# Kernel tuning notes

Measured on AMD Instinct MI355X. Metric: run time of the kernel, lower is better.

## Reference

```python
import jax, jax.numpy as jnp
import numpy as np

Q_DIM, KV_DIM, N_HEAD, C, OUT_DIM, N_AXIS = 256, 256, 8, 32, 256, 1
B, S = 1, 2048

def setup_inputs() -> dict:
    key = jax.random.key(0)
    ks = jax.random.split(key, 9)
    sd = 0.05
    return {
        "q_inputs": jax.random.normal(ks[0], (B, S, Q_DIM), jnp.float32),
        "kv_inputs": jax.random.normal(ks[1], (B, S, KV_DIM), jnp.float32),
        "bias": jax.random.normal(ks[2], (B, N_HEAD, S, S), jnp.float32),
        "qg_weights": jax.random.normal(ks[3], (Q_DIM, N_AXIS, N_HEAD, 2 * C), jnp.float32) * sd,
        "kv_weights": jax.random.normal(ks[4], (KV_DIM, N_AXIS, N_HEAD, 2 * C), jnp.float32) * sd,
        "qg_bias": jax.random.normal(ks[5], (N_AXIS, N_HEAD, 1, 2 * C), jnp.float32) * sd,
        "kv_bias": jax.random.normal(ks[6], (N_AXIS, N_HEAD, 1, 2 * C), jnp.float32) * sd,
        "o_weights": jax.random.normal(ks[7], (N_AXIS, N_HEAD, C, OUT_DIM), jnp.float32) * sd,
        "o_bias": jax.random.normal(ks[8], (OUT_DIM, N_AXIS), jnp.float32) * sd,
    }

def reference(q_inputs, kv_inputs, bias, qg_weights, kv_weights, qg_bias, kv_bias, o_weights, o_bias):
    scale = C ** (-0.5)
    # to_unsqueeze path: add axis dim r (=n_axis=1)
    qi = q_inputs[..., None]          # (B, q, q_dim, r)
    ki = kv_inputs[..., None]         # (B, k, kv_dim, r)
    b = bias[:, None]                 # (B, 1, h, q, k) broadcasts over r
    # per-axis, per-head QKV projections with bias
    qg = jnp.einsum('bqar,arhc->brhqc', qi, qg_weights) + qg_bias
    q, g = jnp.split(qg, 2, axis=-1)  # (B, r, h, q, c) each
    kv = jnp.einsum('bkar,arhc->brhkc', ki, kv_weights) + kv_bias
    k, v = jnp.split(kv, 2, axis=-1)  # (B, r, h, k, c) each
    logits = jnp.einsum('brhqc,brhkc->brhqk', q * scale, k) + b
    attn = jax.nn.softmax(logits, axis=-1)
    attn_out = jnp.einsum('brhqk,brhkc->brhqc', attn, v)
    attn_out = attn_out * jax.nn.sigmoid(g)  # gating
    output = jnp.einsum('brhqc,rhco->bqor', attn_out, o_weights) + o_bias
    return output[..., 0]  # squeeze the n_axis dim (to_unsqueeze path)
```

## Files before the change

### kernel.cpp

```cpp
#include <hip/hip_runtime.h>
#include <hip/hip_bf16.h>
#include <math.h>

#define SEQ   2048
#define NHEAD 8

typedef __attribute__((ext_vector_type(8))) short bf16x8;
typedef __attribute__((ext_vector_type(4))) short bf16x4;
typedef __attribute__((ext_vector_type(4))) float f32x4;

static __device__ __forceinline__ short f2bf(float f) {
    __hip_bfloat16 h = __float2bfloat16(f);
    return *reinterpret_cast<short*>(&h);
}

__global__ __launch_bounds__(256)
void prep_w_kernel(const float* __restrict__ qg_w, const float* __restrict__ kv_w,
                   const float* __restrict__ o_w, short* __restrict__ wqgT,
                   short* __restrict__ wkvT, short* __restrict__ owT)
{
    __shared__ float t[64][65];
    int bid = blockIdx.x;
    const float* src; short* dst; int N, tr, tc;
    if (bid < 32)      { src = qg_w; dst = wqgT; N = 512; tr = bid >> 3; tc = bid & 7; }
    else if (bid < 64) { bid -= 32; src = kv_w; dst = wkvT; N = 512; tr = bid >> 3; tc = bid & 7; }
    else               { bid -= 64; src = o_w;  dst = owT;  N = 256; tr = bid >> 2; tc = bid & 3; }

    const int tid = threadIdx.x;
    const int rr = tid >> 6;
    const int cc = tid & 63;
#pragma unroll
    for (int s = 0; s < 16; s++)
        t[(s << 2) + rr][cc] =
            src[(size_t)((tr << 6) + (s << 2) + rr) * N + (tc << 6) + cc];
    __syncthreads();
#pragma unroll
    for (int s = 0; s < 16; s++)
        dst[(size_t)((tc << 6) + (s << 2) + rr) * 256 + (tr << 6) + cc]
            = f2bf(t[cc][(s << 2) + rr]);
}

__global__ __launch_bounds__(256)
void proj_qgkv_kernel(const float* __restrict__ q_in, const float* __restrict__ kv_in,
                      const short* __restrict__ wqgT, const short* __restrict__ wkvT,
                      const float* __restrict__ qg_b, const float* __restrict__ kv_b,
                      short* __restrict__ qs, float* __restrict__ gs,
                      short* __restrict__ ks, short* __restrict__ vT)
{
    const int z = blockIdx.z;
    const float* __restrict__ A  = z ? kv_in : q_in;
    const short* __restrict__ W  = z ? wkvT : wqgT;
    const float* __restrict__ bv = z ? kv_b : qg_b;

    const int tid = threadIdx.x;
    const int wq = tid >> 6, lane = tid & 63;
    const int ln = lane & 15, quad = lane >> 4;
    const int m0 = blockIdx.x << 6;
    const int n0 = blockIdx.y << 5;

    f32x4 acc[2];
#pragma unroll
    for (int nt = 0; nt < 2; nt++) {
        const float b = bv[n0 + (nt << 4) + ln];
        acc[nt] = (f32x4){b, b, b, b};
    }

    const float* ap = A + (size_t)(m0 + (wq << 4) + ln) * 256 + (quad << 3);
    for (int k8 = 0; k8 < 8; k8++) {
        float4 a0 = *(const float4*)(ap + (k8 << 5));
        float4 a1 = *(const float4*)(ap + (k8 << 5) + 4);
        bf16x8 a;
        a[0] = f2bf(a0.x); a[1] = f2bf(a0.y); a[2] = f2bf(a0.z); a[3] = f2bf(a0.w);
        a[4] = f2bf(a1.x); a[5] = f2bf(a1.y); a[6] = f2bf(a1.z); a[7] = f2bf(a1.w);
#pragma unroll
        for (int nt = 0; nt < 2; nt++) {
            bf16x8 b = *(const bf16x8*)(W + (size_t)(n0 + (nt << 4) + ln) * 256
                                          + (k8 << 5) + (quad << 3));
            acc[nt] = __builtin_amdgcn_mfma_f32_16x16x32_bf16(a, b, acc[nt], 0, 0, 0);
        }
    }

    const float scale = 0.17677669529663689f;
#pragma unroll
    for (int nt = 0; nt < 2; nt++) {
        const int n = n0 + (nt << 4) + ln;
        const int h = n >> 6, c2 = n & 63;
#pragma unroll
        for (int r = 0; r < 4; r++) {
            const int m = m0 + (wq << 4) + (quad << 2) + r;
            const float v = acc[nt][r];
            if (z == 0) {
                if (c2 < 32) qs[(((h << 11) + m) << 5) + c2] = f2bf(v * scale);
                else gs[(((h << 11) + m) << 5) + (c2 - 32)] = 1.0f / (1.0f + __expf(-v));
            } else {
                if (c2 < 32) ks[(((h << 11) + m) << 5) + c2] = f2bf(v);
                else vT[(((h << 5) + (c2 - 32)) << 11) + m] = f2bf(v);
            }
        }
    }
}

__global__ __launch_bounds__(256, 6)
void attn_kernel(const short* __restrict__ qs, const short* __restrict__ ks,
                 const short* __restrict__ vT, const float* __restrict__ bias,
                 float* __restrict__ Opart, float* __restrict__ mpart,
                 float* __restrict__ lpart, int ksize)
{
    const int h = blockIdx.y, z = blockIdx.z;
    const int q0 = blockIdx.x << 6;
    const int tid = threadIdx.x;
    const int wq = tid >> 6, lane = tid & 63;
    const int ln = lane & 15, quad = lane >> 4;

    const int qrow = q0 + (wq << 4) + ln;
    const bf16x8 qf = *(const bf16x8*)(qs + (((size_t)(h << 11) + qrow) << 5) + (quad << 3));

    const float L2E = 1.44269504088896f;
    float ml2 = -1e30f, l = 0.f;
    f32x4 O0 = {0, 0, 0, 0}, O1 = {0, 0, 0, 0};

    const int kbeg  = z * ksize;
    const int ntile = ksize >> 6;
    const float* bp = bias + ((size_t)h * SEQ + qrow) * SEQ + kbeg + (quad << 2);
    const short* kp = ks + (((size_t)(h << 11) + kbeg + ln) << 5) + (quad << 3);

    for (int kt = 0; kt < ntile; kt++) {
        const int k0 = kbeg + (kt << 6);

        f32x4 cb[4];
#pragma unroll
        for (int mt = 0; mt < 4; mt++)
            cb[mt] = *(const f32x4*)(bp + (kt << 6) + (mt << 4));
        bf16x8 kf[4];
#pragma unroll
        for (int mt = 0; mt < 4; mt++)
            kf[mt] = *(const bf16x8*)(kp + (size_t)(((kt << 6) + (mt << 4)) << 5));
        bf16x4 vh[2][2][2];
#pragma unroll
        for (int cm = 0; cm < 2; cm++) {
            const size_t vb = (((size_t)(h << 5) + (cm << 4) + ln) << 11) + k0 + (quad << 2);
#pragma unroll
            for (int kc = 0; kc < 2; kc++)
#pragma unroll
                for (int hf = 0; hf < 2; hf++)
                    vh[cm][kc][hf] = *(const bf16x4*)(vT + vb + (kc << 5) + (hf << 4));
        }

        f32x4 S[4];
#pragma unroll
        for (int mt = 0; mt < 4; mt++)
            S[mt] = __builtin_amdgcn_mfma_f32_16x16x32_bf16(kf[mt], qf, cb[mt], 0, 0, 0);

        float smax = S[0][0];
#pragma unroll
        for (int mt = 0; mt < 4; mt++)
#pragma unroll
            for (int r = 0; r < 4; r++) smax = fmaxf(smax, S[mt][r]);
        smax = fmaxf(smax, __shfl_xor(smax, 16));
        smax = fmaxf(smax, __shfl_xor(smax, 32));
        const float mnew = fmaxf(ml2, smax * L2E);
        const float alpha = exp2f(ml2 - mnew);
        ml2 = mnew;

        float pr[4][4];
        float rs = 0.f;
#pragma unroll
        for (int mt = 0; mt < 4; mt++)
#pragma unroll
            for (int r = 0; r < 4; r++) {
                const float p = exp2f(fmaf(S[mt][r], L2E, -mnew));
                pr[mt][r] = p;
                rs += p;
            }
        rs += __shfl_xor(rs, 16);
        rs += __shfl_xor(rs, 32);
        l = l * alpha + rs;

        short pb[4][4];
#pragma unroll
        for (int mt = 0; mt < 4; mt++)
#pragma unroll
            for (int r = 0; r < 4; r++) pb[mt][r] = f2bf(pr[mt][r]);
        bf16x8 P0 = {pb[0][0], pb[0][1], pb[0][2], pb[0][3],
                     pb[1][0], pb[1][1], pb[1][2], pb[1][3]};
        bf16x8 P1 = {pb[2][0], pb[2][1], pb[2][2], pb[2][3],
                     pb[3][0], pb[3][1], pb[3][2], pb[3][3]};

        O0 *= alpha;
        O1 *= alpha;
#pragma unroll
        for (int kc = 0; kc < 2; kc++) {
            const bf16x8 P = kc ? P1 : P0;
            bf16x8 va0 = __builtin_shufflevector(vh[0][kc][0], vh[0][kc][1],
                                                 0, 1, 2, 3, 4, 5, 6, 7);
            bf16x8 va1 = __builtin_shufflevector(vh[1][kc][0], vh[1][kc][1],
                                                 0, 1, 2, 3, 4, 5, 6, 7);
            O0 = __builtin_amdgcn_mfma_f32_16x16x32_bf16(va0, P, O0, 0, 0, 0);
            O1 = __builtin_amdgcn_mfma_f32_16x16x32_bf16(va1, P, O1, 0, 0, 0);
        }
    }

    const size_t pb_ = (((size_t)(z * NHEAD + h)) << 11) + qrow;
    if (quad == 0) { mpart[pb_] = ml2; lpart[pb_] = l; }
    float* op = Opart + (pb_ << 5);
#pragma unroll
    for (int r = 0; r < 4; r++) {
        op[(quad << 2) + r]      = O0[r];
        op[16 + (quad << 2) + r] = O1[r];
    }
}

__global__ __launch_bounds__(256)
void combine_kernel(const float* __restrict__ Opart, const float* __restrict__ mpart,
                    const float* __restrict__ lpart, const float* __restrict__ gs,
                    short* __restrict__ att, int nsplit)
{
    const int g  = blockIdx.x * 256 + threadIdx.x;
    const int c4 = g & 7;
    const int q  = (g >> 3) & (SEQ - 1);
    const int h  = g >> 14;

    float M = -1e30f;
    for (int s = 0; s < nsplit; s++)
        M = fmaxf(M, mpart[(((size_t)s * NHEAD + h) << 11) + q]);

    float l = 0.f;
    float4 O = {0.f, 0.f, 0.f, 0.f};
    for (int s = 0; s < nsplit; s++) {
        const size_t base = (((size_t)s * NHEAD + h) << 11) + q;
        const float w = exp2f(mpart[base] - M);
        l += w * lpart[base];
        float4 o4 = *(const float4*)(Opart + (base << 5) + (c4 << 2));
        O.x = fmaf(w, o4.x, O.x); O.y = fmaf(w, o4.y, O.y);
        O.z = fmaf(w, o4.z, O.z); O.w = fmaf(w, o4.w, O.w);
    }
    const float inv = 1.0f / l;
    float4 g4 = *(const float4*)(gs + ((((size_t)h << 11) + q) << 5) + (c4 << 2));
    bf16x4 r;
    r[0] = f2bf(O.x * inv * g4.x); r[1] = f2bf(O.y * inv * g4.y);
    r[2] = f2bf(O.z * inv * g4.z); r[3] = f2bf(O.w * inv * g4.w);
    *(bf16x4*)(att + ((size_t)q << 8) + (h << 5) + (c4 << 2)) = r;
}

__global__ __launch_bounds__(256)
void proj_o_kernel(const short* __restrict__ att, const short* __restrict__ owT,
                   const float* __restrict__ o_b, float* __restrict__ out)
{
    const int tid = threadIdx.x;
    const int wq = tid >> 6, lane = tid & 63;
    const int ln = lane & 15, quad = lane >> 4;
    const int m0 = blockIdx.x << 6;
    const int n0 = blockIdx.y << 4;

    const int n = n0 + ln;
    const float b = o_b[n];
    f32x4 acc = (f32x4){b, b, b, b};

    const short* ap = att + (size_t)(m0 + (wq << 4) + ln) * 256 + (quad << 3);
    const short* bp = owT + (size_t)n * 256 + (quad << 3);
#pragma unroll
    for (int k8 = 0; k8 < 8; k8++) {
        bf16x8 a = *(const bf16x8*)(ap + (k8 << 5));
        bf16x8 w = *(const bf16x8*)(bp + (k8 << 5));
        acc = __builtin_amdgcn_mfma_f32_16x16x32_bf16(a, w, acc, 0, 0, 0);
    }
#pragma unroll
    for (int r = 0; r < 4; r++) {
        const int m = m0 + (wq << 4) + (quad << 2) + r;
        out[(size_t)m * 256 + n] = acc[r];
    }
}

extern "C" void kernel_launch(void* const* d_in, const int* in_sizes, int n_in,
                              void* d_out, int out_size, void* d_ws, size_t ws_size,
                              hipStream_t stream)
{
    const float* q_in  = (const float*)d_in[0];
    const float* kv_in = (const float*)d_in[1];
    const float* bias  = (const float*)d_in[2];
    const float* qg_w  = (const float*)d_in[3];
    const float* kv_w  = (const float*)d_in[4];
    const float* qg_b  = (const float*)d_in[5];
    const float* kv_b  = (const float*)d_in[6];
    const float* o_w   = (const float*)d_in[7];
    const float* o_b   = (const float*)d_in[8];
    float* out = (float*)d_out;

    char* p = (char*)d_ws;
    short* qs   = (short*)p; p += 1048576;
    short* ksb  = (short*)p; p += 1048576;
    short* vTb  = (short*)p; p += 1048576;
    short* attb = (short*)p; p += 1048576;
    short* wqgT = (short*)p; p += 262144;
    short* wkvT = (short*)p; p += 262144;
    short* owT  = (short*)p; p += 131072;
    float* gs   = (float*)p; p += 2097152;

    const size_t fixed = (size_t)(p - (char*)d_ws);
    int nsplit = 1;
    {
        const int cand[4] = {8, 4, 2, 1};
        for (int i = 0; i < 4; i++) {
            size_t ns = (size_t)cand[i];
            if (fixed + ns * (size_t)(2097152 + 2 * 65536) <= ws_size) {
                nsplit = cand[i]; break;
            }
        }
    }
    float* mp = (float*)p;
    float* lp = mp + (size_t)nsplit * NHEAD * SEQ;
    float* Op = lp + (size_t)nsplit * NHEAD * SEQ;

    hipLaunchKernelGGL(prep_w_kernel, dim3(80), dim3(256), 0, stream,
                       qg_w, kv_w, o_w, wqgT, wkvT, owT);
    hipLaunchKernelGGL(proj_qgkv_kernel, dim3(32, 16, 2), dim3(256), 0, stream,
                       q_in, kv_in, wqgT, wkvT, qg_b, kv_b, qs, gs, ksb, vTb);
    hipLaunchKernelGGL(attn_kernel, dim3(32, NHEAD, nsplit), dim3(256), 0, stream,
                       qs, ksb, vTb, bias, Op, mp, lp, SEQ / nsplit);
    hipLaunchKernelGGL(combine_kernel, dim3(512), dim3(256), 0, stream,
                       Op, mp, lp, gs, attb, nsplit);
    hipLaunchKernelGGL(proj_o_kernel, dim3(32, 16), dim3(256), 0, stream,
                       attb, owT, o_b, out);
}
```

Baseline: 263.5 us.

## Double-buffer attention loads and pre-pack V into MFMA-fragment layout

The projection kernel now writes V in a packed per-tile layout matching the MFMA operand fragments, so the attention kernel loads V with single 16-byte loads instead of 4-element pieces plus shuffles. The attention loop is templated on tile count and fully unrolled, with register double-buffering of bias, K and V for the next tile, and occupancy hints reduced to 3 blocks to make room for the extra registers. The projection GEMMs also gain register double-buffered loads and vectorized output stores. The aim is to hide global load latency on the bias stream, which dominates memory traffic, at the cost of higher register pressure and lower occupancy.

```diff
diff --git a/kernel.cpp b/kernel.cpp
--- a/kernel.cpp
+++ b/kernel.cpp
@@ -40,12 +40,12 @@
             = f2bf(t[cc][(s << 2) + rr]);
 }
 
-__global__ __launch_bounds__(256)
+__global__ __launch_bounds__(256, 4)
 void proj_qgkv_kernel(const float* __restrict__ q_in, const float* __restrict__ kv_in,
                       const short* __restrict__ wqgT, const short* __restrict__ wkvT,
                       const float* __restrict__ qg_b, const float* __restrict__ kv_b,
                       short* __restrict__ qs, float* __restrict__ gs,
-                      short* __restrict__ ks, short* __restrict__ vT)
+                      short* __restrict__ ks, short* __restrict__ vP)
 {
     const int z = blockIdx.z;
     const float* __restrict__ A  = z ? kv_in : q_in;
@@ -66,18 +66,27 @@
     }
 
     const float* ap = A + (size_t)(m0 + (wq << 4) + ln) * 256 + (quad << 3);
+    const short* wp = W + (size_t)(n0 + ln) * 256 + (quad << 3);
+
+    float4 a4[2][2]; bf16x8 wb[2][2];
+    auto ldp = [&](int b, int k8) {
+        a4[b][0] = *(const float4*)(ap + (k8 << 5));
+        a4[b][1] = *(const float4*)(ap + (k8 << 5) + 4);
+        wb[b][0] = *(const bf16x8*)(wp + (k8 << 5));
+        wb[b][1] = *(const bf16x8*)(wp + 4096 + (k8 << 5));
+    };
+    ldp(0, 0);
+#pragma unroll
     for (int k8 = 0; k8 < 8; k8++) {
-        float4 a0 = *(const float4*)(ap + (k8 << 5));
-        float4 a1 = *(const float4*)(ap + (k8 << 5) + 4);
+        const int b = k8 & 1;
+        if (k8 < 7) ldp(b ^ 1, k8 + 1);
         bf16x8 a;
-        a[0] = f2bf(a0.x); a[1] = f2bf(a0.y); a[2] = f2bf(a0.z); a[3] = f2bf(a0.w);
-        a[4] = f2bf(a1.x); a[5] = f2bf(a1.y); a[6] = f2bf(a1.z); a[7] = f2bf(a1.w);
-#pragma unroll
-        for (int nt = 0; nt < 2; nt++) {
-            bf16x8 b = *(const bf16x8*)(W + (size_t)(n0 + (nt << 4) + ln) * 256
-                                          + (k8 << 5) + (quad << 3));
-            acc[nt] = __builtin_amdgcn_mfma_f32_16x16x32_bf16(a, b, acc[nt], 0, 0, 0);
-        }
+        a[0] = f2bf(a4[b][0].x); a[1] = f2bf(a4[b][0].y);
+        a[2] = f2bf(a4[b][0].z); a[3] = f2bf(a4[b][0].w);
+        a[4] = f2bf(a4[b][1].x); a[5] = f2bf(a4[b][1].y);
+        a[6] = f2bf(a4[b][1].z); a[7] = f2bf(a4[b][1].w);
+        acc[0] = __builtin_amdgcn_mfma_f32_16x16x32_bf16(a, wb[b][0], acc[0], 0, 0, 0);
+        acc[1] = __builtin_amdgcn_mfma_f32_16x16x32_bf16(a, wb[b][1], acc[1], 0, 0, 0);
     }
 
     const float scale = 0.17677669529663689f;
@@ -85,26 +94,40 @@
     for (int nt = 0; nt < 2; nt++) {
         const int n = n0 + (nt << 4) + ln;
         const int h = n >> 6, c2 = n & 63;
-#pragma unroll
-        for (int r = 0; r < 4; r++) {
-            const int m = m0 + (wq << 4) + (quad << 2) + r;
-            const float v = acc[nt][r];
-            if (z == 0) {
+        if (z == 0) {
+#pragma unroll
+            for (int r = 0; r < 4; r++) {
+                const int m = m0 + (wq << 4) + (quad << 2) + r;
+                const float v = acc[nt][r];
                 if (c2 < 32) qs[(((h << 11) + m) << 5) + c2] = f2bf(v * scale);
                 else gs[(((h << 11) + m) << 5) + (c2 - 32)] = 1.0f / (1.0f + __expf(-v));
-            } else {
-                if (c2 < 32) ks[(((h << 11) + m) << 5) + c2] = f2bf(v);
-                else vT[(((h << 5) + (c2 - 32)) << 11) + m] = f2bf(v);
             }
+        } else if (c2 < 32) {
+#pragma unroll
+            for (int r = 0; r < 4; r++) {
+                const int m = m0 + (wq << 4) + (quad << 2) + r;
+                ks[(((h << 11) + m) << 5) + c2] = f2bf(acc[nt][r]);
+            }
+        } else {
+            const int c  = c2 - 32;
+            const int kt = m0 >> 6;
+            const int kc = wq >> 1;
+            const int jb = (wq & 1) << 2;
+            bf16x4 v4;
+            v4[0] = f2bf(acc[nt][0]); v4[1] = f2bf(acc[nt][1]);
+            v4[2] = f2bf(acc[nt][2]); v4[3] = f2bf(acc[nt][3]);
+            *(bf16x4*)(vP + (size_t)((((h << 5) + kt) * 2 + kc) * 4 + quad) * 256
+                          + (c << 3) + jb) = v4;
         }
     }
 }
 
-__global__ __launch_bounds__(256, 6)
+template<int NTILE>
+__global__ __launch_bounds__(256, 3)
 void attn_kernel(const short* __restrict__ qs, const short* __restrict__ ks,
-                 const short* __restrict__ vT, const float* __restrict__ bias,
+                 const short* __restrict__ vP, const float* __restrict__ bias,
                  float* __restrict__ Opart, float* __restrict__ mpart,
-                 float* __restrict__ lpart, int ksize)
+                 float* __restrict__ lpart)
 {
     const int h = blockIdx.y, z = blockIdx.z;
     const int q0 = blockIdx.x << 6;
@@ -119,37 +142,38 @@
     float ml2 = -1e30f, l = 0.f;
     f32x4 O0 = {0, 0, 0, 0}, O1 = {0, 0, 0, 0};
 
-    const int kbeg  = z * ksize;
-    const int ntile = ksize >> 6;
-    const float* bp = bias + ((size_t)h * SEQ + qrow) * SEQ + kbeg + (quad << 2);
-    const short* kp = ks + (((size_t)(h << 11) + kbeg + ln) << 5) + (quad << 3);
-
-    for (int kt = 0; kt < ntile; kt++) {
-        const int k0 = kbeg + (kt << 6);
-
-        f32x4 cb[4];
+    const int kbeg = z * (NTILE << 6);
+    const float* bp  = bias + ((size_t)h * SEQ + qrow) * SEQ + kbeg + (quad << 2);
+    const short* kp  = ks + (((size_t)(h << 11) + kbeg + ln) << 5) + (quad << 3);
+    const short* vp0 = vP + (size_t)((((h << 5) + (kbeg >> 6)) * 2) * 4 + quad) * 256
+                          + (ln << 3);
+
+    f32x4 cb[2][4]; bf16x8 kf[2][4]; bf16x8 vf[2][2][2];
+    auto ld = [&](int b, int t) {
+#pragma unroll
+        for (int mt = 0; mt < 4; mt++) {
+            cb[b][mt] = *(const f32x4*)(bp + (t << 6) + (mt << 4));
+            kf[b][mt] = *(const bf16x8*)(kp + ((size_t)((t << 6) + (mt << 4)) << 5));
+        }
+#pragma unroll
+        for (int kc = 0; kc < 2; kc++)
+#pragma unroll
+            for (int cm = 0; cm < 2; cm++)
+                vf[b][cm][kc] = *(const bf16x8*)(vp0 + (size_t)(t << 11)
+                                                 + (kc << 10) + (cm << 7));
+    };
+
+    ld(0, 0);
+#pragma unroll
+    for (int kt = 0; kt < NTILE; kt++) {
+        const int b = kt & 1;
+        if (kt + 1 < NTILE) ld(b ^ 1, kt + 1);
+
+        f32x4 S[4];
 #pragma unroll
         for (int mt = 0; mt < 4; mt++)
-            cb[mt] = *(const f32x4*)(bp + (kt << 6) + (mt << 4));
-        bf16x8 kf[4];
-#pragma unroll
-        for (int mt = 0; mt < 4; mt++)
-            kf[mt] = *(const bf16x8*)(kp + (size_t)(((kt << 6) + (mt << 4)) << 5));
-        bf16x4 vh[2][2][2];
-#pragma unroll
-        for (int cm = 0; cm < 2; cm++) {
-            const size_t vb = (((size_t)(h << 5) + (cm << 4) + ln) << 11) + k0 + (quad << 2);
-#pragma unroll
-            for (int kc = 0; kc < 2; kc++)
-#pragma unroll
-                for (int hf = 0; hf < 2; hf++)
-                    vh[cm][kc][hf] = *(const bf16x4*)(vT + vb + (kc << 5) + (hf << 4));
-        }
-
-        f32x4 S[4];
-#pragma unroll
-        for (int mt = 0; mt < 4; mt++)
-            S[mt] = __builtin_amdgcn_mfma_f32_16x16x32_bf16(kf[mt], qf, cb[mt], 0, 0, 0);
+            S[mt] = __builtin_amdgcn_mfma_f32_16x16x32_bf16(kf[b][mt], qf,
+                                                            cb[b][mt], 0, 0, 0);
 
         float smax = S[0][0];
 #pragma unroll
@@ -188,26 +212,17 @@
 
         O0 *= alpha;
         O1 *= alpha;
-#pragma unroll
-        for (int kc = 0; kc < 2; kc++) {
-            const bf16x8 P = kc ? P1 : P0;
-            bf16x8 va0 = __builtin_shufflevector(vh[0][kc][0], vh[0][kc][1],
-                                                 0, 1, 2, 3, 4, 5, 6, 7);
-            bf16x8 va1 = __builtin_shufflevector(vh[1][kc][0], vh[1][kc][1],
-                                                 0, 1, 2, 3, 4, 5, 6, 7);
-            O0 = __builtin_amdgcn_mfma_f32_16x16x32_bf16(va0, P, O0, 0, 0, 0);
-            O1 = __builtin_amdgcn_mfma_f32_16x16x32_bf16(va1, P, O1, 0, 0, 0);
-        }
+        O0 = __builtin_amdgcn_mfma_f32_16x16x32_bf16(vf[b][0][0], P0, O0, 0, 0, 0);
+        O1 = __builtin_amdgcn_mfma_f32_16x16x32_bf16(vf[b][1][0], P0, O1, 0, 0, 0);
+        O0 = __builtin_amdgcn_mfma_f32_16x16x32_bf16(vf[b][0][1], P1, O0, 0, 0, 0);
+        O1 = __builtin_amdgcn_mfma_f32_16x16x32_bf16(vf[b][1][1], P1, O1, 0, 0, 0);
     }
 
     const size_t pb_ = (((size_t)(z * NHEAD + h)) << 11) + qrow;
     if (quad == 0) { mpart[pb_] = ml2; lpart[pb_] = l; }
     float* op = Opart + (pb_ << 5);
-#pragma unroll
-    for (int r = 0; r < 4; r++) {
-        op[(quad << 2) + r]      = O0[r];
-        op[16 + (quad << 2) + r] = O1[r];
-    }
+    *(f32x4*)(op + (quad << 2))      = O0;
+    *(f32x4*)(op + 16 + (quad << 2)) = O1;
 }
 
 __global__ __launch_bounds__(256)
@@ -242,7 +257,7 @@
     *(bf16x4*)(att + ((size_t)q << 8) + (h << 5) + (c4 << 2)) = r;
 }
 
-__global__ __launch_bounds__(256)
+__global__ __launch_bounds__(256, 4)
 void proj_o_kernel(const short* __restrict__ att, const short* __restrict__ owT,
                    const float* __restrict__ o_b, float* __restrict__ out)
 {
@@ -258,11 +273,17 @@
 
     const short* ap = att + (size_t)(m0 + (wq << 4) + ln) * 256 + (quad << 3);
     const short* bp = owT + (size_t)n * 256 + (quad << 3);
+
+    bf16x8 a2[2], w2[2];
+    a2[0] = *(const bf16x8*)(ap);  w2[0] = *(const bf16x8*)(bp);
 #pragma unroll
     for (int k8 = 0; k8 < 8; k8++) {
-        bf16x8 a = *(const bf16x8*)(ap + (k8 << 5));
-        bf16x8 w = *(const bf16x8*)(bp + (k8 << 5));
-        acc = __builtin_amdgcn_mfma_f32_16x16x32_bf16(a, w, acc, 0, 0, 0);
+        const int b_ = k8 & 1;
+        if (k8 < 7) {
+            a2[b_ ^ 1] = *(const bf16x8*)(ap + ((k8 + 1) << 5));
+            w2[b_ ^ 1] = *(const bf16x8*)(bp + ((k8 + 1) << 5));
+        }
+        acc = __builtin_amdgcn_mfma_f32_16x16x32_bf16(a2[b_], w2[b_], acc, 0, 0, 0);
     }
 #pragma unroll
     for (int r = 0; r < 4; r++) {
@@ -289,7 +310,7 @@
     char* p = (char*)d_ws;
     short* qs   = (short*)p; p += 1048576;
     short* ksb  = (short*)p; p += 1048576;
-    short* vTb  = (short*)p; p += 1048576;
+    short* vPb  = (short*)p; p += 1048576;
     short* attb = (short*)p; p += 1048576;
     short* wqgT = (short*)p; p += 262144;
     short* wkvT = (short*)p; p += 262144;
@@ -314,9 +335,21 @@
     hipLaunchKernelGGL(prep_w_kernel, dim3(80), dim3(256), 0, stream,
                        qg_w, kv_w, o_w, wqgT, wkvT, owT);
     hipLaunchKernelGGL(proj_qgkv_kernel, dim3(32, 16, 2), dim3(256), 0, stream,
-                       q_in, kv_in, wqgT, wkvT, qg_b, kv_b, qs, gs, ksb, vTb);
-    hipLaunchKernelGGL(attn_kernel, dim3(32, NHEAD, nsplit), dim3(256), 0, stream,
-                       qs, ksb, vTb, bias, Op, mp, lp, SEQ / nsplit);
+                       q_in, kv_in, wqgT, wkvT, qg_b, kv_b, qs, gs, ksb, vPb);
+    switch (nsplit) {
+    case 8:
+        hipLaunchKernelGGL((attn_kernel<4>), dim3(32, NHEAD, 8), dim3(256), 0, stream,
+                           qs, ksb, vPb, bias, Op, mp, lp); break;
+    case 4:
+        hipLaunchKernelGGL((attn_kernel<8>), dim3(32, NHEAD, 4), dim3(256), 0, stream,
+                           qs, ksb, vPb, bias, Op, mp, lp); break;
+    case 2:
+        hipLaunchKernelGGL((attn_kernel<16>), dim3(32, NHEAD, 2), dim3(256), 0, stream,
+                           qs, ksb, vPb, bias, Op, mp, lp); break;
+    default:
+        hipLaunchKernelGGL((attn_kernel<32>), dim3(32, NHEAD, 1), dim3(256), 0, stream,
+                           qs, ksb, vPb, bias, Op, mp, lp); break;
+    }
     hipLaunchKernelGGL(combine_kernel, dim3(512), dim3(256), 0, stream,
                        Op, mp, lp, gs, attb, nsplit);
     hipLaunchKernelGGL(proj_o_kernel, dim3(32, 16), dim3(256), 0, stream,
```

Measured after the change: 248.5 us. 5.7% less time.
